# Performance work log

Measured on AMD Instinct MI355X. Metric: run time of the kernel, lower is better.

## Reference

```python
import jax, jax.numpy as jnp
import numpy as np

BSZ, SEQ, DIM, NH = 2, 2048, 2048, 16
HD = DIM // NH  # 128


def setup_inputs() -> dict:
    key = jax.random.key(0)
    ks = jax.random.split(key, 6)
    x = jax.random.normal(ks[0], (BSZ, SEQ, DIM), dtype=jnp.float32)
    # torch Linear weights: [out_features, in_features]
    scale = 1.0 / np.sqrt(DIM)
    wq = jax.random.normal(ks[1], (DIM, DIM), dtype=jnp.float32) * scale
    wk = jax.random.normal(ks[2], (DIM, DIM), dtype=jnp.float32) * scale
    wv = jax.random.normal(ks[3], (DIM, DIM), dtype=jnp.float32) * scale
    wo = jax.random.normal(ks[4], (DIM, DIM), dtype=jnp.float32) * scale
    # RoPE freqs (llama style): theta=10000
    inv_freq = 1.0 / (10000.0 ** (jnp.arange(0, HD, 2, dtype=jnp.float32) / HD))  # [HD//2]
    t = jnp.arange(SEQ, dtype=jnp.float32)
    angles = jnp.outer(t, inv_freq)  # [SEQ, HD//2]
    freqs_cos = jnp.cos(angles)
    freqs_sin = jnp.sin(angles)
    # causal additive mask [SEQ, SEQ]
    mask = jnp.where(jnp.tril(jnp.ones((SEQ, SEQ), dtype=bool)), 0.0, -jnp.inf).astype(jnp.float32)
    return {"x": x, "wq": wq, "wk": wk, "wv": wv, "wo": wo,
            "freqs_cos": freqs_cos, "freqs_sin": freqs_sin, "mask": mask}


def _apply_rope(v, cos, sin):
    # v: [b, s, h, hd]; complex pairs are interleaved (even=real, odd=imag)
    b, s, h, hd = v.shape
    vr = v.reshape(b, s, h, hd // 2, 2)
    v0, v1 = vr[..., 0], vr[..., 1]
    c = cos[None, :, None, :]  # [1, s, 1, hd//2]
    sn = sin[None, :, None, :]
    out = jnp.stack([v0 * c - v1 * sn, v0 * sn + v1 * c], axis=-1)
    return out.reshape(b, s, h, hd)


def reference(x, wq, wk, wv, wo, freqs_cos, freqs_sin, mask):
    b, s, _ = x.shape
    xq = (x @ wq.T).reshape(b, s, NH, HD)
    xk = (x @ wk.T).reshape(b, s, NH, HD)
    xv = (x @ wv.T).reshape(b, s, NH, HD)
    xq = _apply_rope(xq, freqs_cos, freqs_sin)
    xk = _apply_rope(xk, freqs_cos, freqs_sin)
    # [b, h, s, s]
    scores = jnp.einsum('bqhd,bkhd->bhqk', xq, xk) / jnp.sqrt(jnp.float32(HD))
    scores = scores + mask[None, None, :, :]
    probs = jax.nn.softmax(scores.astype(jnp.float32), axis=-1).astype(scores.dtype)
    out = jnp.einsum('bhqk,bkhd->bqhd', probs, xv).reshape(b, s, NH * HD)
    return out @ wo.T
```

## Files before the change

kernel.cpp:

```cpp
#include <hip/hip_runtime.h>
#include <hip/hip_bf16.h>
#include <stdint.h>

typedef __bf16 bf16x8 __attribute__((ext_vector_type(8)));
typedef float f32x4 __attribute__((ext_vector_type(4)));
typedef unsigned short u16;
typedef unsigned int u32;

#define DEVI __device__ __forceinline__

DEVI u16 f2b(float f){ __bf16 h = (__bf16)f; return __builtin_bit_cast(u16, h); }
DEVI float b2f(u16 u){ return (float)__builtin_bit_cast(__bf16, u); }

constexpr int BSZ = 2, SEQ = 2048, DIM = 2048, NH = 16, HD = 128;

#if defined(__has_builtin)
#if __has_builtin(__builtin_amdgcn_global_load_lds)
#define HAVE_ASYNC_LDS 1
#endif
#endif

DEVI void cp16(void* lds, const void* g){
#ifdef HAVE_ASYNC_LDS
  auto gp = (const __attribute__((address_space(1))) u32*)(uintptr_t)g;
  auto lp = (__attribute__((address_space(3))) u32*)(uintptr_t)lds;
  __builtin_amdgcn_global_load_lds(gp, lp, 16, 0, 0);
#else
  *(uint4*)lds = *(const uint4*)g;
#endif
}

__global__ __launch_bounds__(256) void k_convert(
    const float* __restrict__ x, const float* __restrict__ wq,
    const float* __restrict__ wk, const float* __restrict__ wv,
    const float* __restrict__ wo,
    u16* __restrict__ xb, u16* __restrict__ wqkv, u16* __restrict__ wob)
{
  int e = (blockIdx.x * 256 + threadIdx.x) * 4;
  float4 v; u16* dp;
  if (e < 8388608){
    v = *(const float4*)&x[e]; dp = &xb[e];
  } else if (e < 20971520){
    int o = e - 8388608; int sec = o >> 22; int oo = o & 4194303;
    const float* w = (sec == 0) ? wq : ((sec == 1) ? wk : wv);
    v = *(const float4*)&w[oo]; dp = &wqkv[o];
  } else {
    int o = e - 20971520;
    v = *(const float4*)&wo[o]; dp = &wob[o];
  }
  ushort4 r; r.x = f2b(v.x); r.y = f2b(v.y); r.z = f2b(v.z); r.w = f2b(v.w);
  *(ushort4*)dp = r;
}

DEVI void gemm_core_256x128(u16* smem, const u16* __restrict__ A, const u16* __restrict__ B,
                            int tm, int tn, int t, f32x4 (&acc)[4][4])
{
  const int lane = t & 63, l15 = lane & 15, quad = lane >> 4;
  const int wave = t >> 6, wm = wave >> 1, wn = wave & 1;
  const int swr = (l15 & 7) << 3;
  const int rb = t >> 3;
  const int csw = ((t & 7) ^ (rb & 7)) << 3;
  const u16* As0 = A + (size_t)(tm + rb) * DIM + csw;
  const u16* Bs0 = B + (size_t)(tn + rb) * DIM + csw;

  auto STAGE = [&](int kt){
    const int buf = kt & 1;
    const int kb = kt * 64;
    u16* d = &smem[buf * 24576 + t * 8];
    #pragma unroll
    for (int p = 0; p < 4; ++p)
      cp16(d + p * 4096, As0 + (size_t)p * (64 * DIM) + kb);
    #pragma unroll
    for (int p = 0; p < 2; ++p)
      cp16(d + 16384 + p * 4096, Bs0 + (size_t)p * (64 * DIM) + kb);
  };

  STAGE(0);
  #pragma unroll 2
  for (int kt = 0; kt < DIM / 64; ++kt){
    __syncthreads();
    if (kt < DIM / 64 - 1) STAGE(kt + 1);
    const u16* Ab = &smem[(kt & 1) * 24576];
    const u16* Bb = Ab + 16384;
    bf16x8 Af[4][2], Bf[4][2];
    #pragma unroll
    for (int mt = 0; mt < 4; ++mt)
      #pragma unroll
      for (int ks = 0; ks < 2; ++ks)
        Af[mt][ks] = *(const bf16x8*)&Ab[(wm * 64 + mt * 16 + l15) * 64 + ((ks * 32 + quad * 8) ^ swr)];
    #pragma unroll
    for (int nt = 0; nt < 4; ++nt)
      #pragma unroll
      for (int ks = 0; ks < 2; ++ks)
        Bf[nt][ks] = *(const bf16x8*)&Bb[(wn * 64 + nt * 16 + l15) * 64 + ((ks * 32 + quad * 8) ^ swr)];
    #pragma unroll
    for (int c = 0; c < 4; ++c){
      const int mb = (c >> 1) * 2, nb = (c & 1) * 2;
      __builtin_amdgcn_s_setprio(1);
      #pragma unroll
      for (int mi = 0; mi < 2; ++mi)
        #pragma unroll
        for (int ni = 0; ni < 2; ++ni)
          #pragma unroll
          for (int ks = 0; ks < 2; ++ks)
            acc[mb + mi][nb + ni] = __builtin_amdgcn_mfma_f32_16x16x32_bf16(
                Af[mb + mi][ks], Bf[nb + ni][ks], acc[mb + mi][nb + ni], 0, 0, 0);
      __builtin_amdgcn_s_setprio(0);
    }
  }
  __syncthreads();
}

__global__ __launch_bounds__(512, 2) void k_gemm_qkv(
    const u16* __restrict__ A, const u16* __restrict__ W,
    const float* __restrict__ fc, const float* __restrict__ fs,
    u16* __restrict__ Qd, u16* __restrict__ Kd, u16* __restrict__ Vd)
{
  __shared__ __align__(16) u16 smem[49152];
  const int t = threadIdx.x;
  const int wg = blockIdx.x;
  const int id = (wg & 7) * 96 + (wg >> 3);
  const int tm = (id & 15) << 8;
  const int tn = (id >> 4) << 7;
  f32x4 acc[4][4] = {};
  gemm_core_256x128(smem, A, W, tm, tn, t, acc);

  const int lane = t & 63, l15 = lane & 15, quad = lane >> 4;
  const int wave = t >> 6, wm = wave >> 1, wn = wave & 1;
  u16* Cs = smem;
  #pragma unroll
  for (int mt = 0; mt < 4; ++mt)
    #pragma unroll
    for (int nt = 0; nt < 4; ++nt)
      #pragma unroll
      for (int r = 0; r < 4; ++r){
        int rin = wm * 64 + mt * 16 + quad * 4 + r;
        int col = wn * 64 + nt * 16 + l15;
        Cs[rin * 128 + ((col + rin * 8) & 127)] = f2b(acc[mt][nt][r]);
      }
  __syncthreads();

  const int sec = tn >> 11;
  const int hh = (tn & 2047) >> 7;
  u16* dst = (sec == 0) ? Qd : ((sec == 1) ? Kd : Vd);
  const float qs = (sec == 0) ? (0.08838834764831845f * 1.4426950408889634f) : 1.0f;
  const int col0 = (t & 15) * 8;
  #pragma unroll
  for (int jj = 0; jj < 8; ++jj){
    int row = (t >> 4) + jj * 32;
    int m = tm + row;
    int b = m >> 11, s = m & 2047;
    uint4 cv = *(const uint4*)&Cs[row * 128 + ((col0 + row * 8) & 127)];
    const u16* cp = (const u16*)&cv;
    u16 op[8];
    if (sec < 2){
      float4 c4 = *(const float4*)&fc[(size_t)s * 64 + (col0 >> 1)];
      float4 s4 = *(const float4*)&fs[(size_t)s * 64 + (col0 >> 1)];
      float cc[4] = {c4.x*qs, c4.y*qs, c4.z*qs, c4.w*qs};
      float ss[4] = {s4.x*qs, s4.y*qs, s4.z*qs, s4.w*qs};
      #pragma unroll
      for (int p = 0; p < 4; ++p){
        float a = b2f(cp[2*p]), bb = b2f(cp[2*p+1]);
        op[2*p]   = f2b(a*cc[p] - bb*ss[p]);
        op[2*p+1] = f2b(a*ss[p] + bb*cc[p]);
      }
    } else {
      #pragma unroll
      for (int p = 0; p < 8; ++p) op[p] = cp[p];
    }
    *(uint4*)&dst[((size_t)(b*NH + hh)*SEQ + s)*HD + col0] = *(const uint4*)op;
  }
}

__global__ __launch_bounds__(256) void k_vtrans(
    const u16* __restrict__ V, u16* __restrict__ Vt)
{
  __shared__ u16 ts[64*72];
  const int t = threadIdx.x;
  const int st = blockIdx.x, dt = blockIdx.y, bh = blockIdx.z;
  const size_t base  = (size_t)bh * SEQ * HD;
  const size_t baseT = (size_t)bh * HD * SEQ;
  #pragma unroll
  for (int i = 0; i < 2; ++i){
    int s = i*32 + (t>>3), c = t&7;
    *(uint4*)&ts[s*72 + c*8] = *(const uint4*)&V[base + (size_t)(st*64 + s)*HD + dt*64 + c*8];
  }
  __syncthreads();
  #pragma unroll
  for (int i = 0; i < 2; ++i){
    int d = i*32 + (t>>3), sc = t&7;
    u16 tmp[8];
    #pragma unroll
    for (int j = 0; j < 8; ++j) tmp[j] = ts[(sc*8 + j)*72 + d];
    *(uint4*)&Vt[baseT + (size_t)(dt*64 + d)*SEQ + st*64 + sc*8] = *(const uint4*)tmp;
  }
}

__global__ __launch_bounds__(512) void k_flash(
    const u16* __restrict__ Qd, const u16* __restrict__ Kd,
    const u16* __restrict__ Vt, u16* __restrict__ OP0, u16* __restrict__ OP1,
    float* __restrict__ Mp, float* __restrict__ Lp)
{
  __shared__ __align__(16) u16 lds[40960];
  const int t = threadIdx.x, lane = t & 63, wave = t >> 6;
  const int l15 = lane & 15, quad = lane >> 4;
  const int swz = (l15 & 7) << 3;

  const int flat = blockIdx.x;
  const int xcd = flat & 7, idx = flat >> 3;
  const int bh = xcd * 4 + (idx >> 4);
  const int x = idx & 15;
  const int b = bh >> 4, h = bh & 15;
  const int j = x >> 1, split = x & 1;

  const size_t base  = (size_t)bh * SEQ * HD;
  const size_t baseT = (size_t)bh * HD * SEQ;
  u16* Psw = lds + 32768 + wave * 1024;
  u16* OPs = split ? OP1 : OP0;
  const int lo = 17*split, hi = lo + 17;
  const int qt0 = j, qt1 = 15 - j;
  const int len0 = 2*qt0 + 2;

  const int krow = t >> 4, kslot = t & 15;
  const int vrow = t >> 3, vslot = t & 7;

  for (int pass = 0; pass < 2; ++pass){
    const int qt = pass ? qt1 : qt0;
    const int len = 2*qt + 2;
    int kt0 = pass ? (lo - len0) : lo; if (kt0 < 0) kt0 = 0;
    int kt1 = pass ? (hi - len0) : hi; if (kt1 > len) kt1 = len;
    const int qb = qt*128 + wave*16;

    bf16x8 qf[4];
    #pragma unroll
    for (int ks = 0; ks < 4; ++ks)
      qf[ks] = *(const bf16x8*)&Qd[base + (size_t)(qb + l15)*HD + ks*32 + quad*8];

    f32x4 oacc[8] = {};
    float m_s = -1e30f, l_s = 0.f;

    if (kt0 < kt1){
      uint4 kreg[2], vreg[2];
      auto LOADT = [&](int kt){
        #pragma unroll
        for (int i = 0; i < 2; ++i){
          kreg[i] = *(const uint4*)&Kd[base + (size_t)(kt*64 + i*32 + krow)*HD + kslot*8];
          vreg[i] = *(const uint4*)&Vt[baseT + (size_t)(i*64 + vrow)*SEQ + kt*64 + vslot*8];
        }
      };
      auto WRITET = [&](int bu){
        u16* Kb = lds + bu*8192;
        u16* Vb = lds + 16384 + bu*8192;
        #pragma unroll
        for (int i = 0; i < 2; ++i){
          int kr = i*32 + krow;
          *(uint4*)&Kb[kr*128 + ((kslot*8) ^ ((kr & 7) << 3))] = kreg[i];
          int vr = i*64 + vrow;
          *(uint4*)&Vb[vr*64 + ((vslot*8) ^ ((vr & 7) << 3))] = vreg[i];
        }
      };
      LOADT(kt0);
      WRITET(0);
      if (kt0 + 1 < kt1) LOADT(kt0 + 1);
      __syncthreads();
      int buf = 0;
      for (int kt = kt0; kt < kt1; ++kt){
        if (kt*64 <= qb + 15){
          const u16* Kb = lds + buf*8192;
          const u16* Vb = lds + 16384 + buf*8192;
          f32x4 sacc[4] = {};
          #pragma unroll
          for (int ks = 0; ks < 4; ++ks){
            bf16x8 kf[4];
            #pragma unroll
            for (int nk = 0; nk < 4; ++nk)
              kf[nk] = *(const bf16x8*)&Kb[(nk*16 + l15)*128 + ((ks*32 + quad*8) ^ swz)];
            __builtin_amdgcn_s_setprio(1);
            #pragma unroll
            for (int nk = 0; nk < 4; ++nk)
              sacc[nk] = __builtin_amdgcn_mfma_f32_16x16x32_bf16(kf[nk], qf[ks], sacc[nk], 0, 0, 0);
            __builtin_amdgcn_s_setprio(0);
          }
          if (kt*64 + 63 > qb){
            int q = qb + l15;
            #pragma unroll
            for (int nk = 0; nk < 4; ++nk)
              #pragma unroll
              for (int r = 0; r < 4; ++r){
                int key = kt*64 + nk*16 + quad*4 + r;
                if (key > q) sacc[nk][r] = -1e30f;
              }
          }
          float m4[4];
          #pragma unroll
          for (int nk = 0; nk < 4; ++nk)
            m4[nk] = fmaxf(fmaxf(sacc[nk][0], sacc[nk][1]), fmaxf(sacc[nk][2], sacc[nk][3]));
          float rm = fmaxf(fmaxf(m4[0], m4[1]), fmaxf(m4[2], m4[3]));
          rm = fmaxf(rm, __shfl_xor(rm, 16));
          rm = fmaxf(rm, __shfl_xor(rm, 32));
          float mnew = fmaxf(m_s, rm);
          float alpha = exp2f(m_s - mnew);
          m_s = mnew;
          float s4[4];
          #pragma unroll
          for (int nk = 0; nk < 4; ++nk){
            u16 pk[4];
            float p0 = exp2f(sacc[nk][0] - mnew);
            float p1 = exp2f(sacc[nk][1] - mnew);
            float p2 = exp2f(sacc[nk][2] - mnew);
            float p3 = exp2f(sacc[nk][3] - mnew);
            pk[0] = f2b(p0); pk[1] = f2b(p1); pk[2] = f2b(p2); pk[3] = f2b(p3);
            s4[nk] = (p0 + p1) + (p2 + p3);
            *(uint2*)&Psw[l15*64 + ((nk*16 + quad*4) ^ swz)] = *(const uint2*)pk;
          }
          float rs = (s4[0] + s4[1]) + (s4[2] + s4[3]);
          rs += __shfl_xor(rs, 16);
          rs += __shfl_xor(rs, 32);
          l_s = l_s*alpha + rs;
          #pragma unroll
          for (int db = 0; db < 8; ++db)
            #pragma unroll
            for (int r = 0; r < 4; ++r) oacc[db][r] *= alpha;
          #pragma unroll
          for (int k2 = 0; k2 < 2; ++k2){
            bf16x8 pf = *(const bf16x8*)&Psw[l15*64 + ((k2*32 + quad*8) ^ swz)];
            __builtin_amdgcn_s_setprio(1);
            #pragma unroll
            for (int db = 0; db < 8; ++db){
              bf16x8 vf = *(const bf16x8*)&Vb[(db*16 + l15)*64 + ((k2*32 + quad*8) ^ swz)];
              oacc[db] = __builtin_amdgcn_mfma_f32_16x16x32_bf16(vf, pf, oacc[db], 0, 0, 0);
            }
            __builtin_amdgcn_s_setprio(0);
          }
        }
        if (kt + 1 < kt1){
          WRITET(buf ^ 1);
          if (kt + 2 < kt1) LOADT(kt + 2);
          __syncthreads();
        }
        buf ^= 1;
      }
    }
    {
      u16* Ow = Psw;
      const int qrow = lane >> 2;
      #pragma unroll
      for (int ch = 0; ch < 2; ++ch){
        #pragma unroll
        for (int db2 = 0; db2 < 4; ++db2){
          int db = ch*4 + db2;
          u16 ok[4];
          #pragma unroll
          for (int r = 0; r < 4; ++r) ok[r] = f2b(oacc[db][r]);
          *(uint2*)&Ow[l15*64 + ((db2*16 + quad*4) ^ swz)] = *(const uint2*)ok;
        }
        #pragma unroll
        for (int i = 0; i < 2; ++i){
          int c8 = (lane & 3) + i*4;
          uint4 v = *(const uint4*)&Ow[qrow*64 + ((c8*8) ^ ((qrow & 7) << 3))];
          *(uint4*)&OPs[(((size_t)(b*SEQ + qb + qrow))*NH + h)*HD + ch*64 + c8*8] = v;
        }
      }
      if (quad == 0){
        size_t mi = ((size_t)split*BSZ*NH + bh)*SEQ + (qb + l15);
        Mp[mi] = m_s;
        Lp[mi] = l_s;
      }
    }
    __syncthreads();
  }
}

__global__ __launch_bounds__(256) void k_combine(
    u16* __restrict__ OP0, const u16* __restrict__ OP1,
    const float* __restrict__ Mp, const float* __restrict__ Lp)
{
  size_t flat = ((size_t)blockIdx.x*256 + threadIdx.x)*8;
  int h = (int)((flat >> 7) & 15);
  int s = (int)((flat >> 11) & 2047);
  int b = (int)(flat >> 22);
  size_t row = ((size_t)(b*NH + h))*SEQ + s;
  const size_t off1 = (size_t)BSZ*NH*SEQ;
  float m0 = Mp[row], l0 = Lp[row];
  float m1 = Mp[row + off1], l1 = Lp[row + off1];
  float m = fmaxf(m0, m1);
  float w0 = exp2f(m0 - m), w1 = exp2f(m1 - m);
  float inv = 1.0f / (w0*l0 + w1*l1);
  uint4 a = *(const uint4*)&OP0[flat];
  uint4 c = *(const uint4*)&OP1[flat];
  const u16* pa = (const u16*)&a;
  const u16* pc = (const u16*)&c;
  u16 o[8];
  #pragma unroll
  for (int i = 0; i < 8; ++i)
    o[i] = f2b((b2f(pa[i])*w0 + b2f(pc[i])*w1) * inv);
  *(uint4*)&OP0[flat] = *(const uint4*)o;
}

__global__ __launch_bounds__(512, 2) void k_gemm_out(
    const u16* __restrict__ A, const u16* __restrict__ W, float* __restrict__ out)
{
  __shared__ __align__(16) u16 smem[49152];
  const int t = threadIdx.x;
  const int wg = blockIdx.x;
  const int id = (wg & 7) * 32 + (wg >> 3);
  const int tm = (id & 15) << 8;
  const int tn = (id >> 4) << 7;
  f32x4 acc[4][4] = {};
  gemm_core_256x128(smem, A, W, tm, tn, t, acc);
  const int lane = t & 63, l15 = lane & 15, quad = lane >> 4;
  const int wave = t >> 6, wm = wave >> 1, wn = wave & 1;
  #pragma unroll
  for (int mt = 0; mt < 4; ++mt)
    #pragma unroll
    for (int nt = 0; nt < 4; ++nt)
      #pragma unroll
      for (int r = 0; r < 4; ++r){
        int row = tm + wm*64 + mt*16 + quad*4 + r;
        int col = tn + wn*64 + nt*16 + l15;
        out[(size_t)row*DIM + col] = acc[mt][nt][r];
      }
}

extern "C" void kernel_launch(void* const* d_in, const int* in_sizes, int n_in,
                              void* d_out, int out_size, void* d_ws, size_t ws_size,
                              hipStream_t stream)
{
  const float* x  = (const float*)d_in[0];
  const float* wq = (const float*)d_in[1];
  const float* wk = (const float*)d_in[2];
  const float* wv = (const float*)d_in[3];
  const float* wo = (const float*)d_in[4];
  const float* fc = (const float*)d_in[5];
  const float* fs = (const float*)d_in[6];
  float* out = (float*)d_out;

  char* ws = (char*)d_ws;
  u16* xb   = (u16*)(ws);
  u16* wqkv = (u16*)(ws + 16777216);
  u16* wob  = (u16*)(ws + 41943040);
  u16* Qr   = (u16*)(ws + 50331648);
  u16* Kr   = (u16*)(ws + 67108864);
  u16* Vr   = (u16*)(ws + 83886080);
  u16* Ob   = (u16*)(ws + 100663296);
  u16* VtT  = xb;
  u16* OP1  = wqkv;
  float* Mp = (float*)(ws + 33554432);
  float* Lp = (float*)(ws + 34078720);

  k_convert <<<24576, 256, 0, stream>>>(x, wq, wk, wv, wo, xb, wqkv, wob);
  k_gemm_qkv<<<768, 512, 0, stream>>>(xb, wqkv, fc, fs, Qr, Kr, Vr);
  k_vtrans  <<<dim3(32, 2, 32), 256, 0, stream>>>(Vr, VtT);
  k_flash   <<<512, 512, 0, stream>>>(Qr, Kr, VtT, Ob, OP1, Mp, Lp);
  k_combine <<<4096, 256, 0, stream>>>(Ob, OP1, Mp, Lp);
  k_gemm_out<<<256, 512, 0, stream>>>(Ob, wob, out);
}
```

Before: 439.7 us.

## Fuse V transpose into QKV GEMM epilogue and skip redundant softmax rescale

The QKV GEMM epilogue now writes the V section directly in transposed [b,h,d,s] layout, so the separate k_vtrans kernel and its global round trip go away. In the flash kernel, the running max, the l rescale and the output accumulator rescale are now updated only when some lane's row max increases, checked with a wave ballot. This skips 32 multiplies per tile when the max is stable. In exchange, the V epilogue does strided 16-byte stores along the sequence dimension, and the flash loop gains a data-dependent branch.

New measurement: 429.8 us. -2.3%, faster.

```diff
diff --git a/kernel.cpp b/kernel.cpp
--- a/kernel.cpp
+++ b/kernel.cpp
@@ -114,7 +114,7 @@
 __global__ __launch_bounds__(512, 2) void k_gemm_qkv(
     const u16* __restrict__ A, const u16* __restrict__ W,
     const float* __restrict__ fc, const float* __restrict__ fs,
-    u16* __restrict__ Qd, u16* __restrict__ Kd, u16* __restrict__ Vd)
+    u16* __restrict__ Qd, u16* __restrict__ Kd, u16* __restrict__ Vt)
 {
   __shared__ __align__(16) u16 smem[49152];
   const int t = threadIdx.x;
@@ -142,18 +142,18 @@
 
   const int sec = tn >> 11;
   const int hh = (tn & 2047) >> 7;
-  u16* dst = (sec == 0) ? Qd : ((sec == 1) ? Kd : Vd);
-  const float qs = (sec == 0) ? (0.08838834764831845f * 1.4426950408889634f) : 1.0f;
-  const int col0 = (t & 15) * 8;
-  #pragma unroll
-  for (int jj = 0; jj < 8; ++jj){
-    int row = (t >> 4) + jj * 32;
-    int m = tm + row;
-    int b = m >> 11, s = m & 2047;
-    uint4 cv = *(const uint4*)&Cs[row * 128 + ((col0 + row * 8) & 127)];
-    const u16* cp = (const u16*)&cv;
-    u16 op[8];
-    if (sec < 2){
+  if (sec < 2){
+    u16* dst = (sec == 0) ? Qd : Kd;
+    const float qs = (sec == 0) ? (0.08838834764831845f * 1.4426950408889634f) : 1.0f;
+    const int col0 = (t & 15) * 8;
+    #pragma unroll
+    for (int jj = 0; jj < 8; ++jj){
+      int row = (t >> 4) + jj * 32;
+      int m = tm + row;
+      int b = m >> 11, s = m & 2047;
+      uint4 cv = *(const uint4*)&Cs[row * 128 + ((col0 + row * 8) & 127)];
+      const u16* cp = (const u16*)&cv;
+      u16 op[8];
       float4 c4 = *(const float4*)&fc[(size_t)s * 64 + (col0 >> 1)];
       float4 s4 = *(const float4*)&fs[(size_t)s * 64 + (col0 >> 1)];
       float cc[4] = {c4.x*qs, c4.y*qs, c4.z*qs, c4.w*qs};
@@ -164,35 +164,27 @@
         op[2*p]   = f2b(a*cc[p] - bb*ss[p]);
         op[2*p+1] = f2b(a*ss[p] + bb*cc[p]);
       }
-    } else {
-      #pragma unroll
-      for (int p = 0; p < 8; ++p) op[p] = cp[p];
-    }
-    *(uint4*)&dst[((size_t)(b*NH + hh)*SEQ + s)*HD + col0] = *(const uint4*)op;
-  }
-}
-
-__global__ __launch_bounds__(256) void k_vtrans(
-    const u16* __restrict__ V, u16* __restrict__ Vt)
-{
-  __shared__ u16 ts[64*72];
-  const int t = threadIdx.x;
-  const int st = blockIdx.x, dt = blockIdx.y, bh = blockIdx.z;
-  const size_t base  = (size_t)bh * SEQ * HD;
-  const size_t baseT = (size_t)bh * HD * SEQ;
-  #pragma unroll
-  for (int i = 0; i < 2; ++i){
-    int s = i*32 + (t>>3), c = t&7;
-    *(uint4*)&ts[s*72 + c*8] = *(const uint4*)&V[base + (size_t)(st*64 + s)*HD + dt*64 + c*8];
-  }
-  __syncthreads();
-  #pragma unroll
-  for (int i = 0; i < 2; ++i){
-    int d = i*32 + (t>>3), sc = t&7;
-    u16 tmp[8];
-    #pragma unroll
-    for (int j = 0; j < 8; ++j) tmp[j] = ts[(sc*8 + j)*72 + d];
-    *(uint4*)&Vt[baseT + (size_t)(dt*64 + d)*SEQ + st*64 + sc*8] = *(const uint4*)tmp;
+      *(uint4*)&dst[((size_t)(b*NH + hh)*SEQ + s)*HD + col0] = *(const uint4*)op;
+    }
+  } else {
+    const int bb = tm >> 11;
+    const int sbase = tm & 2047;
+    const size_t baseT = ((size_t)(bb*NH + hh)) * HD * SEQ;
+    const int d0 = (t & 15) * 8;
+    const int s0g = (t >> 4) * 8;
+    u16 tr[8][8];
+    #pragma unroll
+    for (int jr = 0; jr < 8; ++jr){
+      int row = s0g + jr;
+      *(uint4*)&tr[jr][0] = *(const uint4*)&Cs[row * 128 + ((d0 + row * 8) & 127)];
+    }
+    #pragma unroll
+    for (int jd = 0; jd < 8; ++jd){
+      u16 o[8];
+      #pragma unroll
+      for (int jr = 0; jr < 8; ++jr) o[jr] = tr[jr][jd];
+      *(uint4*)&Vt[baseT + (size_t)(d0 + jd)*SEQ + sbase + s0g] = *(const uint4*)o;
+    }
   }
 }
 
@@ -298,17 +290,24 @@
           float rm = fmaxf(fmaxf(m4[0], m4[1]), fmaxf(m4[2], m4[3]));
           rm = fmaxf(rm, __shfl_xor(rm, 16));
           rm = fmaxf(rm, __shfl_xor(rm, 32));
-          float mnew = fmaxf(m_s, rm);
-          float alpha = exp2f(m_s - mnew);
-          m_s = mnew;
+          if (__ballot(rm > m_s) != 0){
+            float mnew = fmaxf(m_s, rm);
+            float alpha = exp2f(m_s - mnew);
+            m_s = mnew;
+            l_s *= alpha;
+            #pragma unroll
+            for (int db = 0; db < 8; ++db)
+              #pragma unroll
+              for (int r = 0; r < 4; ++r) oacc[db][r] *= alpha;
+          }
           float s4[4];
           #pragma unroll
           for (int nk = 0; nk < 4; ++nk){
             u16 pk[4];
-            float p0 = exp2f(sacc[nk][0] - mnew);
-            float p1 = exp2f(sacc[nk][1] - mnew);
-            float p2 = exp2f(sacc[nk][2] - mnew);
-            float p3 = exp2f(sacc[nk][3] - mnew);
+            float p0 = exp2f(sacc[nk][0] - m_s);
+            float p1 = exp2f(sacc[nk][1] - m_s);
+            float p2 = exp2f(sacc[nk][2] - m_s);
+            float p3 = exp2f(sacc[nk][3] - m_s);
             pk[0] = f2b(p0); pk[1] = f2b(p1); pk[2] = f2b(p2); pk[3] = f2b(p3);
             s4[nk] = (p0 + p1) + (p2 + p3);
             *(uint2*)&Psw[l15*64 + ((nk*16 + quad*4) ^ swz)] = *(const uint2*)pk;
@@ -316,11 +315,7 @@
           float rs = (s4[0] + s4[1]) + (s4[2] + s4[3]);
           rs += __shfl_xor(rs, 16);
           rs += __shfl_xor(rs, 32);
-          l_s = l_s*alpha + rs;
-          #pragma unroll
-          for (int db = 0; db < 8; ++db)
-            #pragma unroll
-            for (int r = 0; r < 4; ++r) oacc[db][r] *= alpha;
+          l_s += rs;
           #pragma unroll
           for (int k2 = 0; k2 < 2; ++k2){
             bf16x8 pf = *(const bf16x8*)&Psw[l15*64 + ((k2*32 + quad*8) ^ swz)];
@@ -441,16 +436,14 @@
   u16* wob  = (u16*)(ws + 41943040);
   u16* Qr   = (u16*)(ws + 50331648);
   u16* Kr   = (u16*)(ws + 67108864);
-  u16* Vr   = (u16*)(ws + 83886080);
+  u16* VtT  = (u16*)(ws + 83886080);
   u16* Ob   = (u16*)(ws + 100663296);
-  u16* VtT  = xb;
   u16* OP1  = wqkv;
   float* Mp = (float*)(ws + 33554432);
   float* Lp = (float*)(ws + 34078720);
 
   k_convert <<<24576, 256, 0, stream>>>(x, wq, wk, wv, wo, xb, wqkv, wob);
-  k_gemm_qkv<<<768, 512, 0, stream>>>(xb, wqkv, fc, fs, Qr, Kr, Vr);
-  k_vtrans  <<<dim3(32, 2, 32), 256, 0, stream>>>(Vr, VtT);
+  k_gemm_qkv<<<768, 512, 0, stream>>>(xb, wqkv, fc, fs, Qr, Kr, VtT);
   k_flash   <<<512, 512, 0, stream>>>(Qr, Kr, VtT, Ob, OP1, Mp, Lp);
   k_combine <<<4096, 256, 0, stream>>>(Ob, OP1, Mp, Lp);
   k_gemm_out<<<256, 512, 0, stream>>>(Ob, wob, out);
```
